# Kernel optimization log

Measured on AMD Instinct MI355X. Metric: run time of the kernel, lower is better.

Reference implementation:

```python
import jax, jax.numpy as jnp
import numpy as np

EPS = 1e-5  # clamp floor in BitNet activation quantization


def _bitnet_act_quant(x):
    # Match transformers.integrations.bitnet.ActQuant: per-last-dim int8 fake-quant.
    scale = 127.0 / jnp.clip(jnp.max(jnp.abs(x), axis=-1, keepdims=True), EPS)
    return jnp.clip(jnp.round(x * scale), -128.0, 127.0) / scale


def setup_inputs() -> dict:
    key = jax.random.key(0)
    k1, k2, k3, k4 = jax.random.split(key, 4)
    B, S, D, O = 1, 4096, 4096, 4096  # batch, seq_len, in_features, out_features
    x = jax.random.normal(k1, (B, S, D), dtype=jnp.float32)
    # Ternary weight matrix in {-1, 0, +1} (what the bit-packed RSR format encodes).
    W = jax.random.randint(k2, (O, D), -1, 2).astype(jnp.float32)
    bias = jax.random.normal(k3, (O,), dtype=jnp.float32) * 0.01
    # BitNet weight_scale (divide mode): positive scalar.
    weight_scale = jax.random.uniform(k4, (), dtype=jnp.float32, minval=0.5, maxval=2.0)
    return {"x": x, "W": W, "bias": bias, "weight_scale": weight_scale}


def reference(x, W, bias, weight_scale):
    # CPU backend path: BitNet activation fake-quant, then ternary GEMV per token.
    q = _bitnet_act_quant(x.astype(jnp.float32))
    out = jnp.einsum('bsd,od->bso', q, W)  # [B, S, O]
    out = out + bias
    out = out / weight_scale  # weight_scale_mode == 'divide'
    return out.astype(x.dtype)
```

## Files before the change

### kernel.cpp

```cpp
#include <hip/hip_runtime.h>
#include <hip/hip_bf16.h>


#define SEQ  4096
#define DIM  4096
#define OUTD 4096

typedef int i32x4 __attribute__((ext_vector_type(4)));
typedef unsigned char u8;

__device__ __forceinline__ void gload16(const void* g, void* lds) {
    __builtin_amdgcn_global_load_lds(
        (const __attribute__((address_space(1))) void*)g,
        (__attribute__((address_space(3))) void*)lds, 16, 0, 0);
}

__device__ __forceinline__ int ldsoff(int r, int kq) {
    const int rp = r >> 1;
    const int w = (((r & 1) << 6) | (kq << 4)) ^ ((rp & 3) << 4);
    return rp * 128 + w;
}

__global__ __launch_bounds__(256) void prep_kernel(
    const float* __restrict__ x, char* __restrict__ q, float* __restrict__ rscale,
    const float4* __restrict__ W4, char4* __restrict__ Wb4) {
    const int bid = blockIdx.x;
    const int t = threadIdx.x;
    if (bid < SEQ) {
        const int row = bid;
        const int lane = t & 63, wave = t >> 6;
        const float4* xr = (const float4*)(x + (size_t)row * DIM);
        float4 r[4];
        float m = 0.0f;
#pragma unroll
        for (int i = 0; i < 4; ++i) {
            r[i] = xr[t + 256 * i];
            m = fmaxf(m, fmaxf(fmaxf(fabsf(r[i].x), fabsf(r[i].y)),
                               fmaxf(fabsf(r[i].z), fabsf(r[i].w))));
        }
#pragma unroll
        for (int off = 32; off > 0; off >>= 1)
            m = fmaxf(m, __shfl_xor(m, off, 64));
        __shared__ float red[4];
        if (lane == 0) red[wave] = m;
        __syncthreads();
        const float amax = fmaxf(fmaxf(red[0], red[1]), fmaxf(red[2], red[3]));
        const float scale = 127.0f / fmaxf(amax, 1e-5f);
        if (t == 0) rscale[row] = 1.0f / scale;
        char4* qr = (char4*)(q + (size_t)row * DIM);
#pragma unroll
        for (int i = 0; i < 4; ++i) {
            float q0 = fminf(127.0f, fmaxf(-128.0f, rintf(r[i].x * scale)));
            float q1 = fminf(127.0f, fmaxf(-128.0f, rintf(r[i].y * scale)));
            float q2 = fminf(127.0f, fmaxf(-128.0f, rintf(r[i].z * scale)));
            float q3 = fminf(127.0f, fmaxf(-128.0f, rintf(r[i].w * scale)));
            char4 o;
            o.x = (signed char)q0; o.y = (signed char)q1;
            o.z = (signed char)q2; o.w = (signed char)q3;
            qr[t + 256 * i] = o;
        }
    } else {
        const int n4 = (OUTD * DIM) / 4;
        int i = (bid - SEQ) * 256 + t;
        const int stride = SEQ * 256;
        for (; i < n4; i += stride) {
            float4 w = W4[i];
            char4 o;
            o.x = (signed char)w.x; o.y = (signed char)w.y;
            o.z = (signed char)w.z; o.w = (signed char)w.w;
            Wb4[i] = o;
        }
    }
}

__global__ __launch_bounds__(512, 2) void gemm_kernel(
    const u8* __restrict__ A, const u8* __restrict__ B,
    const float* __restrict__ rscale, const float* __restrict__ bias,
    const float* __restrict__ wscale, float* __restrict__ out) {
    __shared__ __align__(16) u8 As[2 * 2 * 16384];
    __shared__ __align__(16) u8 Bs[2 * 2 * 16384];
    const int tid = threadIdx.x;
    const int lane = tid & 63, wave = tid >> 6;
    const int wr = wave >> 2, wc = wave & 3;
    const int fr = lane & 15, kq = lane >> 4;

    const int bid = blockIdx.x;
    const int swz = (bid & 7) * 32 + (bid >> 3);
    const int brow = swz >> 4, bcol = swz & 15;

    const int v = (tid & 7) ^ ((tid >> 3) & 3);
    const int kb = (v & 3) * 16;
    const int r0 = ((tid >> 3) << 1) + (v >> 2);
    const u8* gA0 = A + (size_t)(brow * 256 + r0) * DIM + kb;
    const u8* gA1 = A + (size_t)(brow * 256 + 128 + r0) * DIM + kb;
    const u8* gB0 = B + (size_t)(bcol * 256 + r0) * DIM + kb;
    const u8* gB1 = B + (size_t)(bcol * 256 + 128 + r0) * DIM + kb;
    u8* lA0 = &As[tid * 16];
    u8* lA1 = &As[8192 + tid * 16];
    u8* lB0 = &Bs[tid * 16];
    u8* lB1 = &Bs[8192 + tid * 16];

#define STAGE(T, S) do {                                                       \
        _Pragma("unroll")                                                      \
        for (int _u = 0; _u < 2; ++_u) {                                       \
            const int _k = (T) * 128 + _u * 64;                                \
            const int _d = (S) * 32768 + _u * 16384;                           \
            gload16(gA0 + _k, lA0 + _d);                                       \
            gload16(gA1 + _k, lA1 + _d);                                       \
            gload16(gB0 + _k, lB0 + _d);                                       \
            gload16(gB1 + _k, lB1 + _d);                                       \
        } } while (0)

    int aoff[8], boff[4];
#pragma unroll
    for (int m = 0; m < 8; ++m) aoff[m] = ldsoff(wr * 128 + m * 16 + fr, kq);
#pragma unroll
    for (int n = 0; n < 4; ++n) boff[n] = ldsoff(wc * 64 + n * 16 + fr, kq);

    i32x4 acc[8][4] = {};

#define COMPUTE(S, U) do {                                                     \
        const int _b = (S) * 32768 + (U) * 16384;                              \
        i32x4 af[8], bfv[4];                                                   \
        _Pragma("unroll")                                                      \
        for (int m = 0; m < 8; ++m)                                            \
            af[m] = *(const i32x4*)&As[_b + aoff[m]];                          \
        _Pragma("unroll")                                                      \
        for (int n = 0; n < 4; ++n)                                            \
            bfv[n] = *(const i32x4*)&Bs[_b + boff[n]];                         \
        _Pragma("unroll")                                                      \
        for (int m = 0; m < 8; ++m)                                            \
            _Pragma("unroll")                                                  \
            for (int n = 0; n < 4; ++n)                                        \
                acc[m][n] = __builtin_amdgcn_mfma_i32_16x16x64_i8(             \
                    af[m], bfv[n], acc[m][n], 0, 0, 0);                        \
    } while (0)

#define VMW(N) asm volatile("s_waitcnt vmcnt(" #N ")" ::: "memory")
#define BAR()  do { asm volatile("" ::: "memory");                             \
                    __builtin_amdgcn_s_barrier();                              \
                    asm volatile("" ::: "memory"); } while (0)

    STAGE(0, 0); STAGE(1, 1);

    for (int tb = 0; tb < 15; ++tb) {
        const int t = tb * 2;
        VMW(8); BAR(); COMPUTE(0, 0); COMPUTE(0, 1); BAR(); STAGE(t + 2, 0);
        VMW(8); BAR(); COMPUTE(1, 0); COMPUTE(1, 1); BAR(); STAGE(t + 3, 1);
    }
    VMW(8); BAR(); COMPUTE(0, 0); COMPUTE(0, 1);
    VMW(0); BAR(); COMPUTE(1, 0); COMPUTE(1, 1);

    const float invws = 1.0f / wscale[0];
    const int rr0 = brow * 256 + wr * 128 + (kq << 2);
    const int c0 = bcol * 256 + wc * 64 + fr;
    float bv[4];
#pragma unroll
    for (int n = 0; n < 4; ++n) bv[n] = bias[c0 + n * 16] * invws;
#pragma unroll
    for (int m = 0; m < 8; ++m) {
#pragma unroll
        for (int j = 0; j < 4; ++j) {
            const int r = rr0 + m * 16 + j;
            const float rs = rscale[r] * invws;
            float* orow = out + (size_t)r * OUTD + c0;
#pragma unroll
            for (int n = 0; n < 4; ++n)
                orow[n * 16] = (float)acc[m][n][j] * rs + bv[n];
        }
    }
#undef STAGE
#undef COMPUTE
#undef VMW
#undef BAR
}

extern "C" void kernel_launch(void* const* d_in, const int* in_sizes, int n_in,
                              void* d_out, int out_size, void* d_ws, size_t ws_size,
                              hipStream_t stream) {
    const float* x      = (const float*)d_in[0];
    const float* W      = (const float*)d_in[1];
    const float* bias   = (const float*)d_in[2];
    const float* wscale = (const float*)d_in[3];
    float* out = (float*)d_out;

    char* ws = (char*)d_ws;
    char* q_i8 = ws;
    char* w_i8 = ws + (size_t)16777216;
    float* rscale = (float*)(ws + (size_t)33554432);

    prep_kernel<<<SEQ + 4096, 256, 0, stream>>>(
        x, q_i8, rscale, (const float4*)W, (char4*)w_i8);
    gemm_kernel<<<256, 512, 0, stream>>>((const u8*)q_i8, (const u8*)w_i8,
                                         rscale, bias, wscale, out);
}
```

Before: 95.43 us.

## Halve GEMM row tile, use triple-buffered 64-wide K stages, double grid

Shrinks the int8 GEMM block tile from 256x256 to 128x256, so the grid grows from 256 to 512 blocks and each wave keeps a 4x4 accumulator set instead of 8x4. The K step drops from 128 to 64 bytes and the two-stage LDS ring becomes a three-stage ring. Each stage's loads are now issued before the compute on the current stage, and the launch-bounds hint now targets four blocks per CU. The aim is to fill all CUs on the MI355X, raise occupancy and hide memory latency better. In exchange, per-tile reuse of the weight operand drops and more barriers run per unit of work.

```diff
diff --git a/kernel.cpp b/kernel.cpp
--- a/kernel.cpp
+++ b/kernel.cpp
@@ -73,63 +73,54 @@
     }
 }
 
-__global__ __launch_bounds__(512, 2) void gemm_kernel(
+__global__ __launch_bounds__(512, 4) void gemm_kernel(
     const u8* __restrict__ A, const u8* __restrict__ B,
     const float* __restrict__ rscale, const float* __restrict__ bias,
     const float* __restrict__ wscale, float* __restrict__ out) {
-    __shared__ __align__(16) u8 As[2 * 2 * 16384];
-    __shared__ __align__(16) u8 Bs[2 * 2 * 16384];
+    __shared__ __align__(16) u8 As[3 * 8192];
+    __shared__ __align__(16) u8 Bs[3 * 16384];
     const int tid = threadIdx.x;
     const int lane = tid & 63, wave = tid >> 6;
     const int wr = wave >> 2, wc = wave & 3;
     const int fr = lane & 15, kq = lane >> 4;
 
     const int bid = blockIdx.x;
-    const int swz = (bid & 7) * 32 + (bid >> 3);
+    const int swz = (bid & 7) * 64 + (bid >> 3);
     const int brow = swz >> 4, bcol = swz & 15;
 
     const int v = (tid & 7) ^ ((tid >> 3) & 3);
     const int kb = (v & 3) * 16;
     const int r0 = ((tid >> 3) << 1) + (v >> 2);
-    const u8* gA0 = A + (size_t)(brow * 256 + r0) * DIM + kb;
-    const u8* gA1 = A + (size_t)(brow * 256 + 128 + r0) * DIM + kb;
+    const u8* gA0 = A + (size_t)(brow * 128 + r0) * DIM + kb;
     const u8* gB0 = B + (size_t)(bcol * 256 + r0) * DIM + kb;
     const u8* gB1 = B + (size_t)(bcol * 256 + 128 + r0) * DIM + kb;
     u8* lA0 = &As[tid * 16];
-    u8* lA1 = &As[8192 + tid * 16];
     u8* lB0 = &Bs[tid * 16];
     u8* lB1 = &Bs[8192 + tid * 16];
 
-#define STAGE(T, S) do {                                                       \
-        _Pragma("unroll")                                                      \
-        for (int _u = 0; _u < 2; ++_u) {                                       \
-            const int _k = (T) * 128 + _u * 64;                                \
-            const int _d = (S) * 32768 + _u * 16384;                           \
-            gload16(gA0 + _k, lA0 + _d);                                       \
-            gload16(gA1 + _k, lA1 + _d);                                       \
-            gload16(gB0 + _k, lB0 + _d);                                       \
-            gload16(gB1 + _k, lB1 + _d);                                       \
-        } } while (0)
+#define STAGE(T, S) do { const int _k = (T) * 64;          \
+        gload16(gA0 + _k, lA0 + (S) * 8192);               \
+        gload16(gB0 + _k, lB0 + (S) * 16384);              \
+        gload16(gB1 + _k, lB1 + (S) * 16384); } while (0)
 
-    int aoff[8], boff[4];
+    int aoff[4], boff[4];
 #pragma unroll
-    for (int m = 0; m < 8; ++m) aoff[m] = ldsoff(wr * 128 + m * 16 + fr, kq);
+    for (int m = 0; m < 4; ++m) aoff[m] = ldsoff(wr * 64 + m * 16 + fr, kq);
 #pragma unroll
     for (int n = 0; n < 4; ++n) boff[n] = ldsoff(wc * 64 + n * 16 + fr, kq);
 
-    i32x4 acc[8][4] = {};
+    i32x4 acc[4][4] = {};
 
-#define COMPUTE(S, U) do {                                                     \
-        const int _b = (S) * 32768 + (U) * 16384;                              \
-        i32x4 af[8], bfv[4];                                                   \
+#define COMPUTE(S) do {                                                        \
+        i32x4 af[4], bfv[4];                                                   \
         _Pragma("unroll")                                                      \
-        for (int m = 0; m < 8; ++m)                                            \
-            af[m] = *(const i32x4*)&As[_b + aoff[m]];                          \
+        for (int m = 0; m < 4; ++m)                                            \
+            af[m] = *(const i32x4*)&As[(S) * 8192 + aoff[m]];                  \
         _Pragma("unroll")                                                      \
         for (int n = 0; n < 4; ++n)                                            \
-            bfv[n] = *(const i32x4*)&Bs[_b + boff[n]];                         \
+            bfv[n] = *(const i32x4*)&Bs[(S) * 16384 + boff[n]];                \
         _Pragma("unroll")                                                      \
-        for (int m = 0; m < 8; ++m)                                            \
+        for (int m = 0; m < 4; ++m)                                            \
             _Pragma("unroll")                                                  \
             for (int n = 0; n < 4; ++n)                                        \
                 acc[m][n] = __builtin_amdgcn_mfma_i32_16x16x64_i8(             \
@@ -143,22 +134,25 @@
 
     STAGE(0, 0); STAGE(1, 1);
 
-    for (int tb = 0; tb < 15; ++tb) {
-        const int t = tb * 2;
-        VMW(8); BAR(); COMPUTE(0, 0); COMPUTE(0, 1); BAR(); STAGE(t + 2, 0);
-        VMW(8); BAR(); COMPUTE(1, 0); COMPUTE(1, 1); BAR(); STAGE(t + 3, 1);
+    for (int tb = 0; tb < 20; ++tb) {
+        const int t = tb * 3;
+        VMW(3); BAR(); STAGE(t + 2, 2); COMPUTE(0);
+        VMW(3); BAR(); STAGE(t + 3, 0); COMPUTE(1);
+        VMW(3); BAR(); STAGE(t + 4, 1); COMPUTE(2);
     }
-    VMW(8); BAR(); COMPUTE(0, 0); COMPUTE(0, 1);
-    VMW(0); BAR(); COMPUTE(1, 0); COMPUTE(1, 1);
+    VMW(3); BAR(); STAGE(62, 2); COMPUTE(0);
+    VMW(3); BAR(); STAGE(63, 0); COMPUTE(1);
+    VMW(3); BAR(); COMPUTE(2);
+    VMW(0); BAR(); COMPUTE(0);
 
     const float invws = 1.0f / wscale[0];
-    const int rr0 = brow * 256 + wr * 128 + (kq << 2);
+    const int rr0 = brow * 128 + wr * 64 + (kq << 2);
     const int c0 = bcol * 256 + wc * 64 + fr;
     float bv[4];
 #pragma unroll
     for (int n = 0; n < 4; ++n) bv[n] = bias[c0 + n * 16] * invws;
 #pragma unroll
-    for (int m = 0; m < 8; ++m) {
+    for (int m = 0; m < 4; ++m) {
 #pragma unroll
         for (int j = 0; j < 4; ++j) {
             const int r = rr0 + m * 16 + j;
@@ -191,6 +185,6 @@
 
     prep_kernel<<<SEQ + 4096, 256, 0, stream>>>(
         x, q_i8, rscale, (const float4*)W, (char4*)w_i8);
-    gemm_kernel<<<256, 512, 0, stream>>>((const u8*)q_i8, (const u8*)w_i8,
+    gemm_kernel<<<512, 512, 0, stream>>>((const u8*)q_i8, (const u8*)w_i8,
                                          rscale, bias, wscale, out);
 }
```

Result: slower. 101.2 us (+6.0%).

## Switch GEMM to 4-stage LDS ring with register double-buffered fragments

Applied to the files above, without the earlier changes.

Restructures the int8 GEMM main loop from two 128-wide K stages to a four-slot ring of 64-wide K stages. Each step issues the next global-to-LDS load, reads the next stage's fragments into a second register set, and runs MFMAs on the current set, with one barrier per 64-K step. The aim is to overlap LDS reads with MFMA work and keep more global loads in flight. In exchange it uses more registers for the two fragment sets, which may hurt occupancy at 2 blocks per CU, and it needs more barriers per unit of K.

```diff
diff --git a/kernel.cpp b/kernel.cpp
--- a/kernel.cpp
+++ b/kernel.cpp
@@ -77,8 +77,8 @@
     const u8* __restrict__ A, const u8* __restrict__ B,
     const float* __restrict__ rscale, const float* __restrict__ bias,
     const float* __restrict__ wscale, float* __restrict__ out) {
-    __shared__ __align__(16) u8 As[2 * 2 * 16384];
-    __shared__ __align__(16) u8 Bs[2 * 2 * 16384];
+    __shared__ __align__(16) u8 As[4 * 16384];
+    __shared__ __align__(16) u8 Bs[4 * 16384];
     const int tid = threadIdx.x;
     const int lane = tid & 63, wave = tid >> 6;
     const int wr = wave >> 2, wc = wave & 3;
@@ -100,16 +100,11 @@
     u8* lB0 = &Bs[tid * 16];
     u8* lB1 = &Bs[8192 + tid * 16];
 
-#define STAGE(T, S) do {                                                       \
-        _Pragma("unroll")                                                      \
-        for (int _u = 0; _u < 2; ++_u) {                                       \
-            const int _k = (T) * 128 + _u * 64;                                \
-            const int _d = (S) * 32768 + _u * 16384;                           \
-            gload16(gA0 + _k, lA0 + _d);                                       \
-            gload16(gA1 + _k, lA1 + _d);                                       \
-            gload16(gB0 + _k, lB0 + _d);                                       \
-            gload16(gB1 + _k, lB1 + _d);                                       \
-        } } while (0)
+#define STAGE(T, S) do { const int _k = (T) * 64;          \
+        gload16(gA0 + _k, lA0 + (S) * 16384);              \
+        gload16(gA1 + _k, lA1 + (S) * 16384);              \
+        gload16(gB0 + _k, lB0 + (S) * 16384);              \
+        gload16(gB1 + _k, lB1 + (S) * 16384); } while (0)
 
     int aoff[8], boff[4];
 #pragma unroll
@@ -119,37 +114,45 @@
 
     i32x4 acc[8][4] = {};
 
-#define COMPUTE(S, U) do {                                                     \
-        const int _b = (S) * 32768 + (U) * 16384;                              \
-        i32x4 af[8], bfv[4];                                                   \
+#define LF(AF, BF, S) do {                                                     \
         _Pragma("unroll")                                                      \
         for (int m = 0; m < 8; ++m)                                            \
-            af[m] = *(const i32x4*)&As[_b + aoff[m]];                          \
+            AF[m] = *(const i32x4*)&As[(S) * 16384 + aoff[m]];                 \
         _Pragma("unroll")                                                      \
         for (int n = 0; n < 4; ++n)                                            \
-            bfv[n] = *(const i32x4*)&Bs[_b + boff[n]];                         \
+            BF[n] = *(const i32x4*)&Bs[(S) * 16384 + boff[n]];                 \
+    } while (0)
+
+#define COMP(AF, BF)                                                           \
+    _Pragma("unroll")                                                          \
+    for (int m = 0; m < 8; ++m)                                                \
         _Pragma("unroll")                                                      \
-        for (int m = 0; m < 8; ++m)                                            \
-            _Pragma("unroll")                                                  \
-            for (int n = 0; n < 4; ++n)                                        \
-                acc[m][n] = __builtin_amdgcn_mfma_i32_16x16x64_i8(             \
-                    af[m], bfv[n], acc[m][n], 0, 0, 0);                        \
-    } while (0)
+        for (int n = 0; n < 4; ++n)                                            \
+            acc[m][n] = __builtin_amdgcn_mfma_i32_16x16x64_i8(                 \
+                AF[m], BF[n], acc[m][n], 0, 0, 0);
 
 #define VMW(N) asm volatile("s_waitcnt vmcnt(" #N ")" ::: "memory")
 #define BAR()  do { asm volatile("" ::: "memory");                             \
                     __builtin_amdgcn_s_barrier();                              \
                     asm volatile("" ::: "memory"); } while (0)
 
-    STAGE(0, 0); STAGE(1, 1);
+    i32x4 fa_a[8], fa_b[4], fb_a[8], fb_b[4];
+
+    STAGE(0, 0); STAGE(1, 1); STAGE(2, 2);
+    VMW(8); BAR();
+    LF(fa_a, fa_b, 0);
 
     for (int tb = 0; tb < 15; ++tb) {
-        const int t = tb * 2;
-        VMW(8); BAR(); COMPUTE(0, 0); COMPUTE(0, 1); BAR(); STAGE(t + 2, 0);
-        VMW(8); BAR(); COMPUTE(1, 0); COMPUTE(1, 1); BAR(); STAGE(t + 3, 1);
+        const int t = tb * 4;
+        VMW(4); BAR(); STAGE(t + 3, 3); LF(fb_a, fb_b, 1); COMP(fa_a, fa_b);
+        VMW(4); BAR(); STAGE(t + 4, 0); LF(fa_a, fa_b, 2); COMP(fb_a, fb_b);
+        VMW(4); BAR(); STAGE(t + 5, 1); LF(fb_a, fb_b, 3); COMP(fa_a, fa_b);
+        VMW(4); BAR(); STAGE(t + 6, 2); LF(fa_a, fa_b, 0); COMP(fb_a, fb_b);
     }
-    VMW(8); BAR(); COMPUTE(0, 0); COMPUTE(0, 1);
-    VMW(0); BAR(); COMPUTE(1, 0); COMPUTE(1, 1);
+    VMW(4); BAR(); STAGE(63, 3); LF(fb_a, fb_b, 1); COMP(fa_a, fa_b);
+    VMW(4); BAR();               LF(fa_a, fa_b, 2); COMP(fb_a, fb_b);
+    VMW(0); BAR();               LF(fb_a, fb_b, 3); COMP(fa_a, fa_b);
+    COMP(fb_a, fb_b);
 
     const float invws = 1.0f / wscale[0];
     const int rr0 = brow * 256 + wr * 128 + (kq << 2);
@@ -170,7 +173,8 @@
         }
     }
 #undef STAGE
-#undef COMPUTE
+#undef LF
+#undef COMP
 #undef VMW
 #undef BAR
 }
```

Result: no change. 96.13 us (+0.7%).
